# Kernel optimization log

Measured on AMD Instinct MI355X. Metric: run time of the kernel, lower is better.

Reference implementation:

```python
import jax, jax.numpy as jnp
import numpy as np

B, N, DV = 32, 1024, 512
L, S, DT = 256, 8, 512
VOCAB = 1024
BAND = 16
LN_EPS = 1e-5


def setup_inputs() -> dict:
    key = jax.random.key(0)
    ks = jax.random.split(key, 12)
    w = lambda k, shp: jax.random.normal(k, shp, dtype=jnp.float32) * 0.02
    return {
        "vis_tokens": jax.random.normal(ks[0], (B, N, DV), dtype=jnp.float32),
        "txt_ctx_ids": jax.random.randint(ks[1], (B, L, S), 0, VOCAB, dtype=jnp.int32),
        "emb_w": w(ks[2], (VOCAB, DT)),        # embedding table, tied with classifier
        "wq": w(ks[3], (DV, DT)),              # q_proj: d_txt -> d_vis
        "wk": w(ks[4], (DV, DV)),
        "wv": w(ks[5], (DV, DV)),
        "wv2t": w(ks[6], (DT, DV)),            # vis2txt: d_vis -> d_txt
        "dw_k": w(ks[7], (DT, 1, 3)),          # depthwise conv1d kernel (O, I/g=1, K)
        "pw_k": w(ks[8], (DT, DT, 1)),         # pointwise conv1d kernel
        "ln_g": jnp.ones((DT,), jnp.float32),
        "ln_b": jnp.zeros((DT,), jnp.float32),
        "dir_alpha": jnp.float32(0.2),
    }


def reference(vis_tokens, txt_ctx_ids, emb_w, wq, wk, wv, wv2t, dw_k, pw_k, ln_g, ln_b, dir_alpha):
    b, n, dv = vis_tokens.shape
    E = emb_w[txt_ctx_ids]                       # [B, L, S, Dt]
    bl = b * E.shape[1]
    x = E.reshape(bl, E.shape[2], DT).transpose(0, 2, 1)  # [B*L, Dt, S]
    dn = ('NCH', 'OIH', 'NCH')
    h = jax.lax.conv_general_dilated(x, dw_k, (1,), 'SAME', dimension_numbers=dn,
                                     feature_group_count=DT)
    y = jax.lax.conv_general_dilated(jax.nn.silu(h), pw_k, (1,), 'SAME', dimension_numbers=dn)
    x = x + y
    m = x.mean(axis=2)                           # [B*L, Dt]
    mu = m.mean(-1, keepdims=True)
    var = ((m - mu) ** 2).mean(-1, keepdims=True)
    q_txt = ((m - mu) * jax.lax.rsqrt(var + LN_EPS) * ln_g + ln_b).reshape(b, -1, DT)  # [B, L, Dt]

    Q = q_txt @ wq.T                             # [B, L, Dv]
    K = vis_tokens @ wk.T                        # [B, N, Dv]
    V = vis_tokens @ wv.T
    logits = jnp.einsum('bld,bnd->bln', Q, K) * (dv ** -0.5)

    # linear centers (torch linspace(0, N-1, L).long() truncates toward zero)
    centers = jnp.linspace(0.0, n - 1, q_txt.shape[1]).astype(jnp.int32)  # [L]
    centers = jnp.broadcast_to(centers[None, :], (b, q_txt.shape[1]))
    idx = jnp.arange(n)[None, None, :]
    signed = (centers[..., None] - idx).astype(jnp.float32)
    logits = logits + dir_alpha * (signed / (BAND + 1e-6))
    keep = jnp.abs(idx - centers[..., None]) <= BAND
    logits = jnp.where(keep, logits, -jnp.inf)

    A = jax.nn.softmax(logits, axis=-1)          # [B, L, N]
    Fv = jnp.einsum('bln,bnd->bld', A, V)        # dropout in source is undefined attr; identity
    H = Fv @ wv2t.T                              # [B, L, Dt]
    cls = H @ emb_w.T                            # tied classifier
    return (cls, H, A)
```

## Files before the change

kernel.cpp:

```cpp
#include <hip/hip_runtime.h>
#include <cmath>

typedef unsigned short u16;
typedef __attribute__((ext_vector_type(8))) short bf16x8;
typedef __attribute__((ext_vector_type(4))) float f32x4;
typedef __attribute__((ext_vector_type(8))) unsigned short u16x8;

#define B_  32
#define N_  1024
#define L_  256
#define S_  8
#define DT_ 512
#define BAND_ 16

__device__ __forceinline__ u16 f2bf(float f) {
  union { float f; unsigned u; } x; x.f = f;
  unsigned r = (x.u + 0x7fffu + ((x.u >> 16) & 1u)) >> 16;
  return (u16)r;
}
__device__ __forceinline__ float bf2f(u16 h) {
  union { unsigned u; float f; } x; x.u = ((unsigned)h) << 16;
  return x.f;
}
__device__ __forceinline__ unsigned cvtpk(float lo, float hi) {
  unsigned r;
  asm volatile("v_cvt_pk_bf16_f32 %0, %1, %2" : "=v"(r) : "v"(lo), "v"(hi));
  return r;
}
__device__ __forceinline__ bf16x8 cvt8(f32x4 a, f32x4 b) {
  union { unsigned u[4]; bf16x8 h; } r;
  r.u[0] = cvtpk(a[0], a[1]); r.u[1] = cvtpk(a[2], a[3]);
  r.u[2] = cvtpk(b[0], b[1]); r.u[3] = cvtpk(b[2], b[3]);
  return r.h;
}

#define B1_WAIT(N)                                       \
  asm volatile("s_waitcnt vmcnt(" #N ")" ::: "memory");  \
  __builtin_amdgcn_s_barrier();                          \
  __builtin_amdgcn_sched_barrier(0);
#define B2_BAR()                                         \
  __builtin_amdgcn_sched_barrier(0);                     \
  __builtin_amdgcn_s_barrier();

__global__ __launch_bounds__(256) void cvt_weights(
    const float* __restrict__ e, const float* __restrict__ q,
    const float* __restrict__ k, const float* __restrict__ v,
    const float* __restrict__ t, const float* __restrict__ pw,
    u16* __restrict__ eo, u16* __restrict__ qo, u16* __restrict__ kvo,
    u16* __restrict__ to, u16* __restrict__ po) {
  int i = blockIdx.x * 256 + threadIdx.x;
  const float* src; u16* dst; int soff, doff;
  if (i < 131072)      { src = e;  dst = eo;  soff = i;          doff = soff; }
  else if (i < 196608) { src = q;  dst = qo;  soff = i - 131072; doff = soff; }
  else if (i < 262144) { src = k;  dst = kvo; soff = i - 196608; doff = soff; }
  else if (i < 327680) { src = v;  dst = kvo; soff = i - 262144; doff = soff + 65536; }
  else if (i < 393216) { src = t;  dst = to;  soff = i - 327680; doff = soff; }
  else                 { src = pw; dst = po;  soff = i - 393216; doff = soff; }
  float4 vv = ((const float4*)src)[soff];
  ushort4 o;
  o.x = f2bf(vv.x); o.y = f2bf(vv.y); o.z = f2bf(vv.z); o.w = f2bf(vv.w);
  ((ushort4*)dst)[doff] = o;
}

__global__ __launch_bounds__(256) void text_front(
    const int* __restrict__ ids, const float* __restrict__ emb,
    const float* __restrict__ dwk, u16* __restrict__ shm,
    float* __restrict__ mbuf) {
  int bl = blockIdx.x;
  int tid = threadIdx.x;
  __shared__ int sid[S_];
  if (tid < S_) sid[tid] = ids[bl * S_ + tid];
  __syncthreads();
  for (int c = tid; c < DT_; c += 256) {
    float x[S_];
#pragma unroll
    for (int s = 0; s < S_; ++s) x[s] = emb[(size_t)sid[s] * DT_ + c];
    float k0 = dwk[c * 3 + 0], k1 = dwk[c * 3 + 1], k2 = dwk[c * 3 + 2];
    float me = 0.f, sh = 0.f;
#pragma unroll
    for (int s = 0; s < S_; ++s) {
      float xm = (s > 0) ? x[s - 1] : 0.0f;
      float xp = (s < S_ - 1) ? x[s + 1] : 0.0f;
      float h = k0 * xm + k1 * x[s] + k2 * xp;
      float si = h / (1.0f + expf(-h));
      me += x[s];
      sh += si;
    }
    shm[(size_t)bl * DT_ + c] = f2bf(sh * (1.0f / S_));
    mbuf[(size_t)bl * DT_ + c] = me * (1.0f / S_);
  }
}

__global__ __launch_bounds__(256, 3) void gemm_kv_f32a(
    const float* __restrict__ A, const u16* __restrict__ B,
    u16* __restrict__ Cb, int M, int N, int K) {
  __shared__ float As[8192];
  __shared__ u16 Bs[8192];
  const int tid = threadIdx.x;
  const int w = tid >> 6;
  const int lane = tid & 63;

  const int gx = gridDim.x;
  const int bid = blockIdx.y * gx + blockIdx.x;
  const int nwg = gx * gridDim.y;
  const int logical = (bid & 7) * (nwg >> 3) + (bid >> 3);
  const int bm = (logical / gx) << 7;
  const int bn = (logical % gx) << 7;
  const int wr = w >> 1, wc = w & 1;

  const int ar0 = (w << 5) + (lane >> 3);
  const int ac = (((lane & 7) ^ ((lane >> 3) & 7)) << 2);
  const float* Ag = A + (size_t)(bm + ar0) * K + ac;

  const int r0 = (w << 4) + (lane >> 2);
  const int kc = (lane & 3) << 3;
  const u16* Bg0 = B + (size_t)(bn + r0) * K + kc;
  const u16* Bg1 = Bg0 + (size_t)64 * K;

  int afo[4][2];
#pragma unroll
  for (int m = 0; m < 4; ++m) {
    const int row = (wr << 6) + (m << 4) + (lane & 15);
#pragma unroll
    for (int c = 0; c < 2; ++c)
      afo[m][c] = (row << 5) + ((((lane >> 4) * 2 + c) ^ (lane & 7)) << 2);
  }
  int boff[4];
#pragma unroll
  for (int n = 0; n < 4; ++n)
    boff[n] = (((wc << 6) + (n << 4) + (lane & 15)) << 5) + ((lane >> 4) << 3);

  f32x4 acc[4][4];
#pragma unroll
  for (int m = 0; m < 4; ++m)
#pragma unroll
    for (int n = 0; n < 4; ++n) acc[m][n] = (f32x4){0.f, 0.f, 0.f, 0.f};

#define STAGE(buf, kt)                                                        \
  {                                                                           \
    float* asb = As + (buf) * 4096 + ((w << 5) << 5);                         \
    _Pragma("unroll")                                                         \
    for (int i = 0; i < 4; ++i) {                                             \
      __builtin_amdgcn_global_load_lds(                                       \
          (const __attribute__((address_space(1))) void*)(Ag + (size_t)(i * 8) * K + (kt)), \
          (__attribute__((address_space(3))) void*)(asb + (i << 8)), 16, 0, 0); \
    }                                                                         \
    u16* bs_ = Bs + (buf) * 4096 + (w << 9);                                  \
    __builtin_amdgcn_global_load_lds(                                         \
        (const __attribute__((address_space(1))) void*)(Bg0 + (kt)),          \
        (__attribute__((address_space(3))) void*)bs_, 16, 0, 0);              \
    __builtin_amdgcn_global_load_lds(                                         \
        (const __attribute__((address_space(1))) void*)(Bg1 + (kt)),          \
        (__attribute__((address_space(3))) void*)(bs_ + 2048), 16, 0, 0);     \
  }

  const int nt = K >> 5;
  STAGE(0, 0);
  int cur = 0;
  for (int t = 0; t < nt; ++t) {
    if (t + 1 < nt) {
      STAGE(cur ^ 1, (t + 1) << 5);
      B1_WAIT(6)
    } else {
      B1_WAIT(0)
    }
    const float* Ab = As + cur * 4096;
    const u16* Bb = Bs + cur * 4096;
    bf16x8 af[4], bfr[4];
#pragma unroll
    for (int m = 0; m < 4; ++m) {
      f32x4 a0 = *(const f32x4*)(Ab + afo[m][0]);
      f32x4 a1 = *(const f32x4*)(Ab + afo[m][1]);
      af[m] = cvt8(a0, a1);
    }
#pragma unroll
    for (int n = 0; n < 4; ++n) bfr[n] = *(const bf16x8*)(Bb + boff[n]);
#pragma unroll
    for (int m = 0; m < 4; ++m)
#pragma unroll
      for (int n = 0; n < 4; ++n)
        acc[m][n] = __builtin_amdgcn_mfma_f32_16x16x32_bf16(
            af[m], bfr[n], acc[m][n], 0, 0, 0);
    B2_BAR()
    cur ^= 1;
  }
#undef STAGE

  const int rb = bm + (wr << 6) + ((lane >> 4) << 2);
  const int cb = bn + (wc << 6) + (lane & 15);
#pragma unroll
  for (int m = 0; m < 4; ++m)
#pragma unroll
    for (int n = 0; n < 4; ++n) {
      int col = cb + (n << 4);
#pragma unroll
      for (int j = 0; j < 4; ++j) {
        size_t idx = (size_t)(rb + (m << 4) + j) * N + col;
        Cb[idx] = f2bf(acc[m][n][j]);
      }
    }
}

template <bool ACC, bool WF32, bool WBF16>
__global__ __launch_bounds__(256) void gemm_mfma(
    const u16* __restrict__ A, const u16* __restrict__ B,
    float* __restrict__ C, u16* __restrict__ Cb, int M, int N, int K) {
  __shared__ u16 As[8192];
  __shared__ u16 Bs[8192];
  const int tid = threadIdx.x;
  const int w = tid >> 6;
  const int lane = tid & 63;

  const int gx = gridDim.x;
  const int bid = blockIdx.y * gx + blockIdx.x;
  const int nwg = gx * gridDim.y;
  const int logical = (bid & 7) * (nwg >> 3) + (bid >> 3);
  const int bm = (logical / gx) << 7;
  const int bn = (logical % gx) << 7;
  const int wr = w >> 1, wc = w & 1;

  const int r0 = (w << 4) + (lane >> 2);
  const int kc = (lane & 3) << 3;
  const u16* Ag0 = A + (size_t)(bm + r0) * K + kc;
  const u16* Ag1 = Ag0 + (size_t)64 * K;
  const u16* Bg0 = B + (size_t)(bn + r0) * K + kc;
  const u16* Bg1 = Bg0 + (size_t)64 * K;

  int aoff[4], boff[4];
#pragma unroll
  for (int m = 0; m < 4; ++m)
    aoff[m] = (((wr << 6) + (m << 4) + (lane & 15)) << 5) + ((lane >> 4) << 3);
#pragma unroll
  for (int n = 0; n < 4; ++n)
    boff[n] = (((wc << 6) + (n << 4) + (lane & 15)) << 5) + ((lane >> 4) << 3);

  f32x4 acc[4][4];
#pragma unroll
  for (int m = 0; m < 4; ++m)
#pragma unroll
    for (int n = 0; n < 4; ++n) acc[m][n] = (f32x4){0.f, 0.f, 0.f, 0.f};

#define STAGE(buf, kt)                                                        \
  {                                                                           \
    u16* as_ = As + (buf) * 4096 + (w << 9);                                  \
    u16* bs_ = Bs + (buf) * 4096 + (w << 9);                                  \
    __builtin_amdgcn_global_load_lds(                                         \
        (const __attribute__((address_space(1))) void*)(Ag0 + (kt)),          \
        (__attribute__((address_space(3))) void*)as_, 16, 0, 0);              \
    __builtin_amdgcn_global_load_lds(                                         \
        (const __attribute__((address_space(1))) void*)(Ag1 + (kt)),          \
        (__attribute__((address_space(3))) void*)(as_ + 2048), 16, 0, 0);     \
    __builtin_amdgcn_global_load_lds(                                         \
        (const __attribute__((address_space(1))) void*)(Bg0 + (kt)),          \
        (__attribute__((address_space(3))) void*)bs_, 16, 0, 0);              \
    __builtin_amdgcn_global_load_lds(                                         \
        (const __attribute__((address_space(1))) void*)(Bg1 + (kt)),          \
        (__attribute__((address_space(3))) void*)(bs_ + 2048), 16, 0, 0);     \
  }

  const int nt = K >> 5;
  STAGE(0, 0);
  int cur = 0;
  for (int t = 0; t < nt; ++t) {
    if (t + 1 < nt) {
      STAGE(cur ^ 1, (t + 1) << 5);
      B1_WAIT(4)
    } else {
      B1_WAIT(0)
    }
    const u16* Ab = As + cur * 4096;
    const u16* Bb = Bs + cur * 4096;
    bf16x8 af[4], bfr[4];
#pragma unroll
    for (int m = 0; m < 4; ++m) af[m] = *(const bf16x8*)(Ab + aoff[m]);
#pragma unroll
    for (int n = 0; n < 4; ++n) bfr[n] = *(const bf16x8*)(Bb + boff[n]);
#pragma unroll
    for (int m = 0; m < 4; ++m)
#pragma unroll
      for (int n = 0; n < 4; ++n)
        acc[m][n] = __builtin_amdgcn_mfma_f32_16x16x32_bf16(
            af[m], bfr[n], acc[m][n], 0, 0, 0);
    B2_BAR()
    cur ^= 1;
  }
#undef STAGE

  const int rb = bm + (wr << 6) + ((lane >> 4) << 2);
  const int cb = bn + (wc << 6) + (lane & 15);
#pragma unroll
  for (int m = 0; m < 4; ++m)
#pragma unroll
    for (int n = 0; n < 4; ++n) {
      int col = cb + (n << 4);
#pragma unroll
      for (int j = 0; j < 4; ++j) {
        size_t idx = (size_t)(rb + (m << 4) + j) * N + col;
        float v = acc[m][n][j];
        if (ACC) v += C[idx];
        if (WF32) C[idx] = v;
        if (WBF16) Cb[idx] = f2bf(v);
      }
    }
}

template <bool ACC, bool WF32, bool WBF16>
__global__ __launch_bounds__(256) void gemm_n64(
    const u16* __restrict__ A, const u16* __restrict__ B,
    float* __restrict__ C, u16* __restrict__ Cb, int M, int N, int K) {
  __shared__ u16 As[8192];
  __shared__ u16 Bs[4096];
  const int tid = threadIdx.x;
  const int w = tid >> 6;
  const int lane = tid & 63;

  const int gx = gridDim.x;
  const int bid = blockIdx.y * gx + blockIdx.x;
  const int nwg = gx * gridDim.y;
  const int logical = (bid & 7) * (nwg >> 3) + (bid >> 3);
  const int bm = (logical / gx) << 7;
  const int bn = (logical % gx) << 6;

  const int r0 = (w << 4) + (lane >> 2);
  const int kc = (lane & 3) << 3;
  const u16* Ag0 = A + (size_t)(bm + r0) * K + kc;
  const u16* Ag1 = Ag0 + (size_t)64 * K;
  const u16* Bg0 = B + (size_t)(bn + r0) * K + kc;

  int aoff[2], boff[4];
#pragma unroll
  for (int m = 0; m < 2; ++m)
    aoff[m] = (((w << 5) + (m << 4) + (lane & 15)) << 5) + ((lane >> 4) << 3);
#pragma unroll
  for (int n = 0; n < 4; ++n)
    boff[n] = (((n << 4) + (lane & 15)) << 5) + ((lane >> 4) << 3);

  f32x4 acc[2][4];
#pragma unroll
  for (int m = 0; m < 2; ++m)
#pragma unroll
    for (int n = 0; n < 4; ++n) acc[m][n] = (f32x4){0.f, 0.f, 0.f, 0.f};

#define STAGE(buf, kt)                                                        \
  {                                                                           \
    u16* as_ = As + (buf) * 4096 + (w << 9);                                  \
    u16* bs_ = Bs + (buf) * 2048 + (w << 9);                                  \
    __builtin_amdgcn_global_load_lds(                                         \
        (const __attribute__((address_space(1))) void*)(Ag0 + (kt)),          \
        (__attribute__((address_space(3))) void*)as_, 16, 0, 0);              \
    __builtin_amdgcn_global_load_lds(                                         \
        (const __attribute__((address_space(1))) void*)(Ag1 + (kt)),          \
        (__attribute__((address_space(3))) void*)(as_ + 2048), 16, 0, 0);     \
    __builtin_amdgcn_global_load_lds(                                         \
        (const __attribute__((address_space(1))) void*)(Bg0 + (kt)),          \
        (__attribute__((address_space(3))) void*)bs_, 16, 0, 0);              \
  }

  const int nt = K >> 5;
  STAGE(0, 0);
  int cur = 0;
  for (int t = 0; t < nt; ++t) {
    if (t + 1 < nt) {
      STAGE(cur ^ 1, (t + 1) << 5);
      B1_WAIT(3)
    } else {
      B1_WAIT(0)
    }
    const u16* Ab = As + cur * 4096;
    const u16* Bb = Bs + cur * 2048;
    bf16x8 af[2], bfr[4];
#pragma unroll
    for (int m = 0; m < 2; ++m) af[m] = *(const bf16x8*)(Ab + aoff[m]);
#pragma unroll
    for (int n = 0; n < 4; ++n) bfr[n] = *(const bf16x8*)(Bb + boff[n]);
#pragma unroll
    for (int m = 0; m < 2; ++m)
#pragma unroll
      for (int n = 0; n < 4; ++n)
        acc[m][n] = __builtin_amdgcn_mfma_f32_16x16x32_bf16(
            af[m], bfr[n], acc[m][n], 0, 0, 0);
    B2_BAR()
    cur ^= 1;
  }
#undef STAGE

  const int rb = bm + (w << 5) + ((lane >> 4) << 2);
  const int cb = bn + (lane & 15);
#pragma unroll
  for (int m = 0; m < 2; ++m)
#pragma unroll
    for (int n = 0; n < 4; ++n) {
      int col = cb + (n << 4);
#pragma unroll
      for (int j = 0; j < 4; ++j) {
        size_t idx = (size_t)(rb + (m << 4) + j) * N + col;
        float v = acc[m][n][j];
        if (ACC) v += C[idx];
        if (WF32) C[idx] = v;
        if (WBF16) Cb[idx] = f2bf(v);
      }
    }
}

__global__ __launch_bounds__(256) void ln_kernel(
    const float* __restrict__ m, const float* __restrict__ g,
    const float* __restrict__ bta, u16* __restrict__ q) {
  int row = blockIdx.x;
  int tid = threadIdx.x;
  float v0 = m[(size_t)row * 512 + tid];
  float v1 = m[(size_t)row * 512 + 256 + tid];
  __shared__ float red[4], red2[4];
  float s = v0 + v1;
#pragma unroll
  for (int d = 32; d; d >>= 1) s += __shfl_xor(s, d);
  if ((tid & 63) == 0) red[tid >> 6] = s;
  __syncthreads();
  float mu = (red[0] + red[1] + red[2] + red[3]) * (1.0f / 512.0f);
  float d0 = v0 - mu, d1 = v1 - mu;
  float s2 = d0 * d0 + d1 * d1;
#pragma unroll
  for (int d = 32; d; d >>= 1) s2 += __shfl_xor(s2, d);
  if ((tid & 63) == 0) red2[tid >> 6] = s2;
  __syncthreads();
  float var = (red2[0] + red2[1] + red2[2] + red2[3]) * (1.0f / 512.0f);
  float r = rsqrtf(var + 1e-5f);
  q[(size_t)row * 512 + tid] = f2bf(d0 * r * g[tid] + bta[tid]);
  q[(size_t)row * 512 + 256 + tid] = f2bf(d1 * r * g[tid + 256] + bta[tid + 256]);
}

__global__ __launch_bounds__(512) void attn_kernel(
    const u16* __restrict__ Qb, const u16* __restrict__ KV,
    const float* __restrict__ alpha_p, float* __restrict__ A,
    u16* __restrict__ Fv) {
  __shared__ u16 KV_s[96 * 512];
  __shared__ u16 Q_s[16 * 520];
  __shared__ float S_s[16 * 100];

  const int bid = blockIdx.x;
  const int logical = (bid & 7) * 64 + (bid >> 3);
  const int b = logical >> 4, lg = logical & 15;
  const int l0 = lg * 16;
  const int tid = threadIdx.x;
  const int w = tid >> 6, lane = tid & 63;
  const float al = *alpha_p;

  const int c_min = (1023 * l0) / 255;
  const int kb0 = min(max(c_min - BAND_, 0), N_ - 96);

  {
    const size_t rowb = (size_t)(b * N_ + kb0);
    for (int rr = 0; rr < 12; ++rr) {
      const int r = w * 12 + rr;
      const u16* src = KV + (rowb + r) * 1024 + ((lane * 8) ^ ((r & 7) << 3));
      u16* dst = KV_s + r * 512;
      __builtin_amdgcn_global_load_lds(
          (const __attribute__((address_space(1))) void*)src,
          (__attribute__((address_space(3))) void*)dst, 16, 0, 0);
    }
  }
  {
    const int r = tid >> 5;
    const u16* qrow = Qb + (size_t)(b * L_ + l0 + r) * 512;
#pragma unroll
    for (int h = 0; h < 2; ++h) {
      const int ch = (tid & 31) + h * 32;
      u16x8 v = *(const u16x8*)(qrow + ch * 8);
      *(u16x8*)(Q_s + r * 520 + ch * 8) = v;
    }
  }
  __syncthreads();

  if (w < 6) {
    f32x4 acc = {0.f, 0.f, 0.f, 0.f};
    const int arow = (lane & 15) * 520 + ((lane >> 4) << 3);
    const int key = w * 16 + (lane & 15);
    const int swz = (key & 7) << 3;
    for (int ks = 0; ks < 16; ++ks) {
      bf16x8 aq = *(const bf16x8*)(Q_s + arow + ks * 32);
      bf16x8 bk =
          *(const bf16x8*)(KV_s + key * 512 + ((ks * 32 + ((lane >> 4) << 3)) ^ swz));
      acc = __builtin_amdgcn_mfma_f32_16x16x32_bf16(aq, bk, acc, 0, 0, 0);
    }
#pragma unroll
    for (int j = 0; j < 4; ++j)
      S_s[((lane >> 4) * 4 + j) * 100 + w * 16 + (lane & 15)] = acc[j];
  }
  __syncthreads();

  {
    const size_t rowb = (size_t)(b * N_ + kb0);
    for (int rr = 0; rr < 12; ++rr) {
      const int r = w * 12 + rr;
      const u16* src =
          KV + (rowb + r) * 1024 + 512 + ((lane * 8) ^ ((r & 7) << 3));
      u16* dst = KV_s + r * 512;
      __builtin_amdgcn_global_load_lds(
          (const __attribute__((address_space(1))) void*)src,
          (__attribute__((address_space(3))) void*)dst, 16, 0, 0);
    }
  }

#pragma unroll
  for (int rr = 0; rr < 2; ++rr) {
    const int l = 2 * w + rr;
    const int c = (1023 * (l0 + l)) / 255;
    const int g0 = kb0 + lane, g1 = kb0 + 64 + lane;
    const bool v0 = (g0 >= c - BAND_) && (g0 <= c + BAND_);
    const bool v1 = (lane < 32) && (g1 >= c - BAND_) && (g1 <= c + BAND_);
    const float sc = 0.044194173824159216f;
    float x0 = v0 ? S_s[l * 100 + lane] * sc +
                        al * ((float)(c - g0) * (1.0f / 16.000001f))
                  : -INFINITY;
    float x1 = v1 ? S_s[l * 100 + 64 + lane] * sc +
                        al * ((float)(c - g1) * (1.0f / 16.000001f))
                  : -INFINITY;
    float mx = fmaxf(x0, x1);
#pragma unroll
    for (int d = 32; d; d >>= 1) mx = fmaxf(mx, __shfl_xor(mx, d));
    float e0 = v0 ? expf(x0 - mx) : 0.0f;
    float e1 = v1 ? expf(x1 - mx) : 0.0f;
    float sm = e0 + e1;
#pragma unroll
    for (int d = 32; d; d >>= 1) sm += __shfl_xor(sm, d);
    const float inv = 1.0f / sm;
    S_s[l * 100 + lane] = e0 * inv;
    if (lane < 32) S_s[l * 100 + 64 + lane] = e1 * inv;
    const int lo = max(0, c - BAND_), hi = min(N_ - 1, c + BAND_);
    float* Arow = A + (size_t)(b * L_ + l0 + l) * N_;
#pragma unroll
    for (int p4 = 0; p4 < 4; ++p4) {
      const int p = (p4 * 64 + lane) * 4;
      float4 v;
      v.x = (p + 0 >= lo && p + 0 <= hi) ? S_s[l * 100 + p + 0 - kb0] : 0.0f;
      v.y = (p + 1 >= lo && p + 1 <= hi) ? S_s[l * 100 + p + 1 - kb0] : 0.0f;
      v.z = (p + 2 >= lo && p + 2 <= hi) ? S_s[l * 100 + p + 2 - kb0] : 0.0f;
      v.w = (p + 3 >= lo && p + 3 <= hi) ? S_s[l * 100 + p + 3 - kb0] : 0.0f;
      ((float4*)Arow)[p4 * 64 + lane] = v;
    }
  }
  __syncthreads();

#pragma unroll
  for (int rr = 0; rr < 2; ++rr) {
    const int l = 2 * w + rr;
    const int c = (1023 * (l0 + l)) / 255;
    const int jlo = max(0, c - BAND_) - kb0, jhi = min(N_ - 1, c + BAND_) - kb0;
    float acc[8] = {};
    for (int j = jlo; j <= jhi; ++j) {
      const float avj = S_s[l * 100 + j];
      const u16x8 v =
          *(const u16x8*)(KV_s + j * 512 + ((lane * 8) ^ ((j & 7) << 3)));
#pragma unroll
      for (int t = 0; t < 8; ++t) acc[t] += avj * bf2f(v[t]);
    }
    u16x8 fo;
#pragma unroll
    for (int t = 0; t < 8; ++t) fo[t] = f2bf(acc[t]);
    *(u16x8*)(Fv + (size_t)(b * L_ + l0 + l) * 512 + lane * 8) = fo;
  }
}

extern "C" void kernel_launch(void* const* d_in, const int* in_sizes, int n_in,
                              void* d_out, int out_size, void* d_ws,
                              size_t ws_size, hipStream_t stream) {
  const float* vis = (const float*)d_in[0];
  const int* ids = (const int*)d_in[1];
  const float* emb = (const float*)d_in[2];
  const float* wq = (const float*)d_in[3];
  const float* wk = (const float*)d_in[4];
  const float* wvp = (const float*)d_in[5];
  const float* wv2t = (const float*)d_in[6];
  const float* dwk = (const float*)d_in[7];
  const float* pwk = (const float*)d_in[8];
  const float* lng = (const float*)d_in[9];
  const float* lnb = (const float*)d_in[10];
  const float* alpha = (const float*)d_in[11];

  float* out_cls = (float*)d_out;
  float* out_H = out_cls + (size_t)8192 * 1024;
  float* out_A = out_H + (size_t)8192 * 512;

  char* p = (char*)d_ws;
  u16* KVb  = (u16*)p;              p += (size_t)32768 * 1024 * 2;
  u16* embb = (u16*)p;              p += (size_t)1024 * 512 * 2;
  u16* wqb  = (u16*)p;              p += (size_t)512 * 512 * 2;
  u16* wkvb = (u16*)p;              p += (size_t)1024 * 512 * 2;
  u16* wv2tb= (u16*)p;              p += (size_t)512 * 512 * 2;
  u16* pwkb = (u16*)p;              p += (size_t)512 * 512 * 2;
  u16* shmb = (u16*)p;              p += (size_t)8192 * 512 * 2;
  float* mbuf = (float*)p;          p += (size_t)8192 * 512 * 4;
  u16* qbuf = (u16*)p;              p += (size_t)8192 * 512 * 2;
  u16* Qbf  = (u16*)p;              p += (size_t)8192 * 512 * 2;
  u16* Fvb  = (u16*)p;              p += (size_t)8192 * 512 * 2;
  u16* Hb   = (u16*)p;              p += (size_t)8192 * 512 * 2;

  cvt_weights<<<1792, 256, 0, stream>>>(emb, wq, wk, wvp, wv2t, pwk,
                                        embb, wqb, wkvb, wv2tb, pwkb);

  gemm_kv_f32a<<<dim3(8, 256), 256, 0, stream>>>(
      vis, wkvb, KVb, 32768, 1024, 512);

  text_front<<<8192, 256, 0, stream>>>(ids, emb, dwk, shmb, mbuf);
  gemm_n64<true, true, false><<<dim3(8, 64), 256, 0, stream>>>(
      shmb, pwkb, mbuf, nullptr, 8192, 512, 512);
  ln_kernel<<<8192, 256, 0, stream>>>(mbuf, lng, lnb, qbuf);
  gemm_n64<false, false, true><<<dim3(8, 64), 256, 0, stream>>>(
      qbuf, wqb, nullptr, Qbf, 8192, 512, 512);
  attn_kernel<<<512, 512, 0, stream>>>(Qbf, KVb, alpha, out_A, Fvb);
  gemm_n64<false, true, true><<<dim3(8, 64), 256, 0, stream>>>(
      Fvb, wv2tb, out_H, Hb, 8192, 512, 512);
  gemm_mfma<false, true, false><<<dim3(8, 64), 256, 0, stream>>>(
      Hb, embb, out_cls, nullptr, 8192, 1024, 512);
}
```

Before: 219.4 us.

## Convert A to bf16 in registers before LDS in K/V projection GEMM

In the K/V projection GEMM, the fp32 A operand is no longer streamed straight into LDS with global_load_lds. Each thread now loads it into registers two tiles ahead, packs it to bf16 and writes the packed values to a bf16 LDS buffer. The aim is to halve A's LDS footprint and read traffic and to take the per-MFMA conversion out of the compute loop. The cost is more VGPRs for the staging registers and a manual vmcnt/lgkmcnt schedule. The launch-bounds occupancy hint is dropped, the loop is unrolled by two and assumes an even tile count, and the new LDS writes are unswizzled, which may cause bank conflicts.

```diff
diff --git a/kernel.cpp b/kernel.cpp
--- a/kernel.cpp
+++ b/kernel.cpp
@@ -26,12 +26,6 @@
   unsigned r;
   asm volatile("v_cvt_pk_bf16_f32 %0, %1, %2" : "=v"(r) : "v"(lo), "v"(hi));
   return r;
-}
-__device__ __forceinline__ bf16x8 cvt8(f32x4 a, f32x4 b) {
-  union { unsigned u[4]; bf16x8 h; } r;
-  r.u[0] = cvtpk(a[0], a[1]); r.u[1] = cvtpk(a[2], a[3]);
-  r.u[2] = cvtpk(b[0], b[1]); r.u[3] = cvtpk(b[2], b[3]);
-  return r.h;
 }
 
 #define B1_WAIT(N)                                       \
@@ -91,10 +85,10 @@
   }
 }
 
-__global__ __launch_bounds__(256, 3) void gemm_kv_f32a(
+__global__ __launch_bounds__(256) void gemm_kv_f32a(
     const float* __restrict__ A, const u16* __restrict__ B,
     u16* __restrict__ Cb, int M, int N, int K) {
-  __shared__ float As[8192];
+  __shared__ u16 As[8192];
   __shared__ u16 Bs[8192];
   const int tid = threadIdx.x;
   const int w = tid >> 6;
@@ -108,24 +102,20 @@
   const int bn = (logical % gx) << 7;
   const int wr = w >> 1, wc = w & 1;
 
-  const int ar0 = (w << 5) + (lane >> 3);
-  const int ac = (((lane & 7) ^ ((lane >> 3) & 7)) << 2);
-  const float* Ag = A + (size_t)(bm + ar0) * K + ac;
+  const int arow = tid & 127;
+  const int akh = tid >> 7;
+  const float* Ap = A + (size_t)(bm + arow) * K + akh * 16;
+  const int awoff = arow * 32 + akh * 16;
 
   const int r0 = (w << 4) + (lane >> 2);
   const int kc = (lane & 3) << 3;
   const u16* Bg0 = B + (size_t)(bn + r0) * K + kc;
   const u16* Bg1 = Bg0 + (size_t)64 * K;
 
-  int afo[4][2];
-#pragma unroll
-  for (int m = 0; m < 4; ++m) {
-    const int row = (wr << 6) + (m << 4) + (lane & 15);
-#pragma unroll
-    for (int c = 0; c < 2; ++c)
-      afo[m][c] = (row << 5) + ((((lane >> 4) * 2 + c) ^ (lane & 7)) << 2);
-  }
-  int boff[4];
+  int aoff[4], boff[4];
+#pragma unroll
+  for (int m = 0; m < 4; ++m)
+    aoff[m] = (((wr << 6) + (m << 4) + (lane & 15)) << 5) + ((lane >> 4) << 3);
 #pragma unroll
   for (int n = 0; n < 4; ++n)
     boff[n] = (((wc << 6) + (n << 4) + (lane & 15)) << 5) + ((lane >> 4) << 3);
@@ -136,15 +126,29 @@
 #pragma unroll
     for (int n = 0; n < 4; ++n) acc[m][n] = (f32x4){0.f, 0.f, 0.f, 0.f};
 
-#define STAGE(buf, kt)                                                        \
+  float4 sreg[2][4];
+
+#define LOADA(P, kt)                                \
+  sreg[P][0] = *(const float4*)(Ap + (kt));         \
+  sreg[P][1] = *(const float4*)(Ap + (kt) + 4);     \
+  sreg[P][2] = *(const float4*)(Ap + (kt) + 8);     \
+  sreg[P][3] = *(const float4*)(Ap + (kt) + 12);
+#define WRITEA(buf, P)                                                        \
   {                                                                           \
-    float* asb = As + (buf) * 4096 + ((w << 5) << 5);                         \
-    _Pragma("unroll")                                                         \
-    for (int i = 0; i < 4; ++i) {                                             \
-      __builtin_amdgcn_global_load_lds(                                       \
-          (const __attribute__((address_space(1))) void*)(Ag + (size_t)(i * 8) * K + (kt)), \
-          (__attribute__((address_space(3))) void*)(asb + (i << 8)), 16, 0, 0); \
-    }                                                                         \
+    uint4 q0, q1;                                                             \
+    q0.x = cvtpk(sreg[P][0].x, sreg[P][0].y);                                 \
+    q0.y = cvtpk(sreg[P][0].z, sreg[P][0].w);                                 \
+    q0.z = cvtpk(sreg[P][1].x, sreg[P][1].y);                                 \
+    q0.w = cvtpk(sreg[P][1].z, sreg[P][1].w);                                 \
+    q1.x = cvtpk(sreg[P][2].x, sreg[P][2].y);                                 \
+    q1.y = cvtpk(sreg[P][2].z, sreg[P][2].w);                                 \
+    q1.z = cvtpk(sreg[P][3].x, sreg[P][3].y);                                 \
+    q1.w = cvtpk(sreg[P][3].z, sreg[P][3].w);                                 \
+    *(uint4*)(As + (buf) * 4096 + awoff) = q0;                                \
+    *(uint4*)(As + (buf) * 4096 + awoff + 8) = q1;                            \
+  }
+#define STAGEB(buf, kt)                                                       \
+  {                                                                           \
     u16* bs_ = Bs + (buf) * 4096 + (w << 9);                                  \
     __builtin_amdgcn_global_load_lds(                                         \
         (const __attribute__((address_space(1))) void*)(Bg0 + (kt)),          \
@@ -153,38 +157,59 @@
         (const __attribute__((address_space(1))) void*)(Bg1 + (kt)),          \
         (__attribute__((address_space(3))) void*)(bs_ + 2048), 16, 0, 0);     \
   }
+#define COMPUTE(buf)                                                          \
+  {                                                                           \
+    const u16* Ab = As + (buf) * 4096;                                        \
+    const u16* Bb = Bs + (buf) * 4096;                                        \
+    bf16x8 af[4], bfr[4];                                                     \
+    _Pragma("unroll")                                                         \
+    for (int m = 0; m < 4; ++m) af[m] = *(const bf16x8*)(Ab + aoff[m]);       \
+    _Pragma("unroll")                                                         \
+    for (int n = 0; n < 4; ++n) bfr[n] = *(const bf16x8*)(Bb + boff[n]);      \
+    _Pragma("unroll")                                                         \
+    for (int m = 0; m < 4; ++m)                                               \
+      _Pragma("unroll")                                                       \
+      for (int n = 0; n < 4; ++n)                                             \
+        acc[m][n] = __builtin_amdgcn_mfma_f32_16x16x32_bf16(                  \
+            af[m], bfr[n], acc[m][n], 0, 0, 0);                               \
+  }
+#define ITER(tt, PL, PW, BUFC, BUFN)                                          \
+  {                                                                           \
+    if ((tt) + 2 < nt) { LOADA(PL, ((tt) + 2) << 5) }                         \
+    if ((tt) + 1 < nt) { STAGEB(BUFN, ((tt) + 1) << 5) }                      \
+    if ((tt) + 2 < nt) {                                                      \
+      asm volatile("s_waitcnt vmcnt(6)" ::: "memory");                        \
+    } else if ((tt) + 1 < nt) {                                               \
+      asm volatile("s_waitcnt vmcnt(2)" ::: "memory");                        \
+    } else {                                                                  \
+      asm volatile("s_waitcnt vmcnt(0)" ::: "memory");                        \
+    }                                                                         \
+    __builtin_amdgcn_sched_barrier(0);                                        \
+    if ((tt) + 1 < nt) { WRITEA(BUFN, PW) }                                   \
+    asm volatile("s_waitcnt lgkmcnt(0)" ::: "memory");                        \
+    __builtin_amdgcn_s_barrier();                                             \
+    __builtin_amdgcn_sched_barrier(0);                                        \
+    COMPUTE(BUFC)                                                             \
+    B2_BAR()                                                                  \
+  }
 
   const int nt = K >> 5;
-  STAGE(0, 0);
-  int cur = 0;
-  for (int t = 0; t < nt; ++t) {
-    if (t + 1 < nt) {
-      STAGE(cur ^ 1, (t + 1) << 5);
-      B1_WAIT(6)
-    } else {
-      B1_WAIT(0)
-    }
-    const float* Ab = As + cur * 4096;
-    const u16* Bb = Bs + cur * 4096;
-    bf16x8 af[4], bfr[4];
-#pragma unroll
-    for (int m = 0; m < 4; ++m) {
-      f32x4 a0 = *(const f32x4*)(Ab + afo[m][0]);
-      f32x4 a1 = *(const f32x4*)(Ab + afo[m][1]);
-      af[m] = cvt8(a0, a1);
-    }
-#pragma unroll
-    for (int n = 0; n < 4; ++n) bfr[n] = *(const bf16x8*)(Bb + boff[n]);
-#pragma unroll
-    for (int m = 0; m < 4; ++m)
-#pragma unroll
-      for (int n = 0; n < 4; ++n)
-        acc[m][n] = __builtin_amdgcn_mfma_f32_16x16x32_bf16(
-            af[m], bfr[n], acc[m][n], 0, 0, 0);
-    B2_BAR()
-    cur ^= 1;
-  }
-#undef STAGE
+  LOADA(0, 0)
+  LOADA(1, 32)
+  STAGEB(0, 0)
+  asm volatile("s_waitcnt vmcnt(6)" ::: "memory");
+  __builtin_amdgcn_sched_barrier(0);
+  WRITEA(0, 0)
+
+  for (int t = 0; t + 1 < nt; t += 2) {
+    ITER(t, 0, 1, 0, 1)
+    ITER(t + 1, 1, 0, 1, 0)
+  }
+#undef ITER
+#undef COMPUTE
+#undef STAGEB
+#undef WRITEA
+#undef LOADA
 
   const int rb = bm + (wr << 6) + ((lane >> 4) << 2);
   const int cb = bn + (wc << 6) + (lane & 15);
```

New measurement: 257.3 us. 1.17x slower.

## Pre-convert vis tokens to bf16 and use 256x256 four-stage KV GEMM

Applied to the files above, without the earlier changes.

Adds a separate kernel that converts vis_tokens to bf16 in workspace, so the KV projection no longer loads fp32 A tiles and converts them inside the GEMM loop. The KV GEMM is replaced with a 512-thread, 256x256-tile kernel using a four-buffer global_load_lds pipeline, a swizzled bf16 LDS layout and raised wave priority around the MFMA blocks. This cuts per-tile conversion work and raises data reuse per block. In exchange it adds an extra pass that writes and rereads a 32 MB bf16 copy, uses 128 KB of LDS per block (lower occupancy), and the grid shrinks to 512 blocks.

```diff
diff --git a/kernel.cpp b/kernel.cpp
--- a/kernel.cpp
+++ b/kernel.cpp
@@ -21,17 +21,6 @@
 __device__ __forceinline__ float bf2f(u16 h) {
   union { unsigned u; float f; } x; x.u = ((unsigned)h) << 16;
   return x.f;
-}
-__device__ __forceinline__ unsigned cvtpk(float lo, float hi) {
-  unsigned r;
-  asm volatile("v_cvt_pk_bf16_f32 %0, %1, %2" : "=v"(r) : "v"(lo), "v"(hi));
-  return r;
-}
-__device__ __forceinline__ bf16x8 cvt8(f32x4 a, f32x4 b) {
-  union { unsigned u[4]; bf16x8 h; } r;
-  r.u[0] = cvtpk(a[0], a[1]); r.u[1] = cvtpk(a[2], a[3]);
-  r.u[2] = cvtpk(b[0], b[1]); r.u[3] = cvtpk(b[2], b[3]);
-  return r.h;
 }
 
 #define B1_WAIT(N)                                       \
@@ -41,6 +30,17 @@
 #define B2_BAR()                                         \
   __builtin_amdgcn_sched_barrier(0);                     \
   __builtin_amdgcn_s_barrier();
+
+__global__ __launch_bounds__(256) void cvt_bf16(
+    const float* __restrict__ in, u16* __restrict__ out, int n4) {
+  int i = blockIdx.x * 256 + threadIdx.x;
+  if (i < n4) {
+    float4 v = ((const float4*)in)[i];
+    ushort4 o;
+    o.x = f2bf(v.x); o.y = f2bf(v.y); o.z = f2bf(v.z); o.w = f2bf(v.w);
+    ((ushort4*)out)[i] = o;
+  }
+}
 
 __global__ __launch_bounds__(256) void cvt_weights(
     const float* __restrict__ e, const float* __restrict__ q,
@@ -91,108 +91,120 @@
   }
 }
 
-__global__ __launch_bounds__(256, 3) void gemm_kv_f32a(
-    const float* __restrict__ A, const u16* __restrict__ B,
+__global__ __launch_bounds__(512) void gemm_kv_8ph(
+    const u16* __restrict__ A, const u16* __restrict__ B,
     u16* __restrict__ Cb, int M, int N, int K) {
-  __shared__ float As[8192];
-  __shared__ u16 Bs[8192];
+  __shared__ u16 As[32768];
+  __shared__ u16 Bs[32768];
   const int tid = threadIdx.x;
   const int w = tid >> 6;
   const int lane = tid & 63;
+  const int wm = w >> 2, wn = w & 3;
 
   const int gx = gridDim.x;
   const int bid = blockIdx.y * gx + blockIdx.x;
   const int nwg = gx * gridDim.y;
   const int logical = (bid & 7) * (nwg >> 3) + (bid >> 3);
-  const int bm = (logical / gx) << 7;
-  const int bn = (logical % gx) << 7;
-  const int wr = w >> 1, wc = w & 1;
-
-  const int ar0 = (w << 5) + (lane >> 3);
-  const int ac = (((lane & 7) ^ ((lane >> 3) & 7)) << 2);
-  const float* Ag = A + (size_t)(bm + ar0) * K + ac;
-
-  const int r0 = (w << 4) + (lane >> 2);
-  const int kc = (lane & 3) << 3;
-  const u16* Bg0 = B + (size_t)(bn + r0) * K + kc;
-  const u16* Bg1 = Bg0 + (size_t)64 * K;
-
-  int afo[4][2];
-#pragma unroll
-  for (int m = 0; m < 4; ++m) {
-    const int row = (wr << 6) + (m << 4) + (lane & 15);
-#pragma unroll
-    for (int c = 0; c < 2; ++c)
-      afo[m][c] = (row << 5) + ((((lane >> 4) * 2 + c) ^ (lane & 7)) << 2);
-  }
-  int boff[4];
-#pragma unroll
-  for (int n = 0; n < 4; ++n)
-    boff[n] = (((wc << 6) + (n << 4) + (lane & 15)) << 5) + ((lane >> 4) << 3);
-
-  f32x4 acc[4][4];
-#pragma unroll
-  for (int m = 0; m < 4; ++m)
+  const int bm = (logical / gx) << 8;
+  const int bn = (logical % gx) << 8;
+
+  const int rowS0 = (w << 5) + (lane >> 2);
+  const int rowS1 = rowS0 + 16;
+  const int gac = (((lane & 3) ^ ((lane >> 3) & 3)) << 3);
+  const u16* AgS0 = A + (size_t)(bm + rowS0) * K + gac;
+  const u16* AgS1 = A + (size_t)(bm + rowS1) * K + gac;
+  const u16* BgS0 = B + (size_t)(bn + rowS0) * K + gac;
+  const u16* BgS1 = B + (size_t)(bn + rowS1) * K + gac;
+  const int ldsS0 = (w << 10) + 0;
+  const int ldsS1 = (w << 10) + 512;
+
+#define STAGE(step)                                                           \
+  {                                                                           \
+    const int bufo_ = ((step) & 3) << 13;                                     \
+    const int ks_ = (step) << 5;                                              \
+    __builtin_amdgcn_global_load_lds(                                         \
+        (const __attribute__((address_space(1))) void*)(AgS0 + ks_),          \
+        (__attribute__((address_space(3))) void*)(As + bufo_ + ldsS0), 16, 0, 0); \
+    __builtin_amdgcn_global_load_lds(                                         \
+        (const __attribute__((address_space(1))) void*)(AgS1 + ks_),          \
+        (__attribute__((address_space(3))) void*)(As + bufo_ + ldsS1), 16, 0, 0); \
+    __builtin_amdgcn_global_load_lds(                                         \
+        (const __attribute__((address_space(1))) void*)(BgS0 + ks_),          \
+        (__attribute__((address_space(3))) void*)(Bs + bufo_ + ldsS0), 16, 0, 0); \
+    __builtin_amdgcn_global_load_lds(                                         \
+        (const __attribute__((address_space(1))) void*)(BgS1 + ks_),          \
+        (__attribute__((address_space(3))) void*)(Bs + bufo_ + ldsS1), 16, 0, 0); \
+  }
+
+  const int kg = lane >> 4;
+  int aoff[8], boff[4];
+#pragma unroll
+  for (int m = 0; m < 8; ++m) {
+    const int r = (wm << 7) + (m << 4) + (lane & 15);
+    aoff[m] = (r << 5) + ((kg ^ ((r >> 1) & 3)) << 3);
+  }
+#pragma unroll
+  for (int n = 0; n < 4; ++n) {
+    const int r = (wn << 6) + (n << 4) + (lane & 15);
+    boff[n] = (r << 5) + ((kg ^ ((r >> 1) & 3)) << 3);
+  }
+
+  f32x4 acc[8][4];
+#pragma unroll
+  for (int m = 0; m < 8; ++m)
 #pragma unroll
     for (int n = 0; n < 4; ++n) acc[m][n] = (f32x4){0.f, 0.f, 0.f, 0.f};
 
-#define STAGE(buf, kt)                                                        \
+#define GROUP_BODY(sbuf)                                                      \
   {                                                                           \
-    float* asb = As + (buf) * 4096 + ((w << 5) << 5);                         \
+    const u16* Ab = As + ((sbuf) << 13);                                      \
+    const u16* Bb = Bs + ((sbuf) << 13);                                      \
+    bf16x8 af[8], bfr[4];                                                     \
     _Pragma("unroll")                                                         \
-    for (int i = 0; i < 4; ++i) {                                             \
-      __builtin_amdgcn_global_load_lds(                                       \
-          (const __attribute__((address_space(1))) void*)(Ag + (size_t)(i * 8) * K + (kt)), \
-          (__attribute__((address_space(3))) void*)(asb + (i << 8)), 16, 0, 0); \
-    }                                                                         \
-    u16* bs_ = Bs + (buf) * 4096 + (w << 9);                                  \
-    __builtin_amdgcn_global_load_lds(                                         \
-        (const __attribute__((address_space(1))) void*)(Bg0 + (kt)),          \
-        (__attribute__((address_space(3))) void*)bs_, 16, 0, 0);              \
-    __builtin_amdgcn_global_load_lds(                                         \
-        (const __attribute__((address_space(1))) void*)(Bg1 + (kt)),          \
-        (__attribute__((address_space(3))) void*)(bs_ + 2048), 16, 0, 0);     \
+    for (int m = 0; m < 8; ++m) af[m] = *(const bf16x8*)(Ab + aoff[m]);       \
+    _Pragma("unroll")                                                         \
+    for (int n = 0; n < 4; ++n) bfr[n] = *(const bf16x8*)(Bb + boff[n]);      \
+    asm volatile("s_waitcnt lgkmcnt(0)" ::: "memory");                        \
+    __builtin_amdgcn_sched_barrier(0);                                        \
+    __builtin_amdgcn_s_setprio(1);                                            \
+    _Pragma("unroll")                                                         \
+    for (int m = 0; m < 8; ++m)                                               \
+      _Pragma("unroll")                                                       \
+      for (int n = 0; n < 4; ++n)                                             \
+        acc[m][n] = __builtin_amdgcn_mfma_f32_16x16x32_bf16(                  \
+            af[m], bfr[n], acc[m][n], 0, 0, 0);                               \
+    __builtin_amdgcn_s_setprio(0);                                            \
   }
 
   const int nt = K >> 5;
-  STAGE(0, 0);
-  int cur = 0;
-  for (int t = 0; t < nt; ++t) {
-    if (t + 1 < nt) {
-      STAGE(cur ^ 1, (t + 1) << 5);
-      B1_WAIT(6)
-    } else {
-      B1_WAIT(0)
-    }
-    const float* Ab = As + cur * 4096;
-    const u16* Bb = Bs + cur * 4096;
-    bf16x8 af[4], bfr[4];
-#pragma unroll
-    for (int m = 0; m < 4; ++m) {
-      f32x4 a0 = *(const f32x4*)(Ab + afo[m][0]);
-      f32x4 a1 = *(const f32x4*)(Ab + afo[m][1]);
-      af[m] = cvt8(a0, a1);
-    }
-#pragma unroll
-    for (int n = 0; n < 4; ++n) bfr[n] = *(const bf16x8*)(Bb + boff[n]);
-#pragma unroll
-    for (int m = 0; m < 4; ++m)
-#pragma unroll
-      for (int n = 0; n < 4; ++n)
-        acc[m][n] = __builtin_amdgcn_mfma_f32_16x16x32_bf16(
-            af[m], bfr[n], acc[m][n], 0, 0, 0);
-    B2_BAR()
-    cur ^= 1;
-  }
+  STAGE(0)
+  STAGE(1)
+  STAGE(2)
+  for (int s = 0; s <= nt - 4; ++s) {
+    __builtin_amdgcn_s_barrier();
+    STAGE(s + 3)
+    B1_WAIT(12)
+    GROUP_BODY(s & 3)
+  }
+  __builtin_amdgcn_s_barrier();
+  B1_WAIT(8)
+  GROUP_BODY((nt - 3) & 3)
+  __builtin_amdgcn_s_barrier();
+  B1_WAIT(4)
+  GROUP_BODY((nt - 2) & 3)
+  __builtin_amdgcn_s_barrier();
+  B1_WAIT(0)
+  GROUP_BODY((nt - 1) & 3)
+#undef GROUP_BODY
 #undef STAGE
 
-  const int rb = bm + (wr << 6) + ((lane >> 4) << 2);
-  const int cb = bn + (wc << 6) + (lane & 15);
-#pragma unroll
-  for (int m = 0; m < 4; ++m)
+  const int rb = bm + (wm << 7) + ((lane >> 4) << 2);
+  const int cb = bn + (wn << 6) + (lane & 15);
+#pragma unroll
+  for (int m = 0; m < 8; ++m)
 #pragma unroll
     for (int n = 0; n < 4; ++n) {
-      int col = cb + (n << 4);
+      const int col = cb + (n << 4);
 #pragma unroll
       for (int j = 0; j < 4; ++j) {
         size_t idx = (size_t)(rb + (m << 4) + j) * N + col;
@@ -581,6 +593,7 @@
   float* out_A = out_H + (size_t)8192 * 512;
 
   char* p = (char*)d_ws;
+  u16* visb = (u16*)p;              p += (size_t)32768 * 512 * 2;
   u16* KVb  = (u16*)p;              p += (size_t)32768 * 1024 * 2;
   u16* embb = (u16*)p;              p += (size_t)1024 * 512 * 2;
   u16* wqb  = (u16*)p;              p += (size_t)512 * 512 * 2;
@@ -594,11 +607,12 @@
   u16* Fvb  = (u16*)p;              p += (size_t)8192 * 512 * 2;
   u16* Hb   = (u16*)p;              p += (size_t)8192 * 512 * 2;
 
+  cvt_bf16<<<16384, 256, 0, stream>>>(vis, visb, 32768 * 512 / 4);
   cvt_weights<<<1792, 256, 0, stream>>>(emb, wq, wk, wvp, wv2t, pwk,
                                         embb, wqb, wkvb, wv2tb, pwkb);
 
-  gemm_kv_f32a<<<dim3(8, 256), 256, 0, stream>>>(
-      vis, wkvb, KVb, 32768, 1024, 512);
+  gemm_kv_8ph<<<dim3(4, 128), 512, 0, stream>>>(
+      visb, wkvb, KVb, 32768, 1024, 512);
 
   text_front<<<8192, 256, 0, stream>>>(ids, emb, dwk, shmb, mbuf);
   gemm_n64<true, true, false><<<dim3(8, 64), 256, 0, stream>>>(
```

Measured after the change: 211.8 us. 1.04x faster.
